# Kernel tuning notes

Hardware: AMD Instinct MI355X
Metric: run time of the kernel (lower is better)

The kernel has to match this reference:

```python
import jax, jax.numpy as jnp
import numpy as np

N = 8192        # num_drugs
D_EMB = 256     # args.gcn_hidden3 (global encoder input)
D_FEAT = 256    # args.hidden_size (local encoder input)
H1 = H2 = H3 = 256  # args.ff_hidden1/2/3
LOG2 = float(np.log(2.0))
ADJ_DENSITY = 0.01


def _ff(x, w1, b1, w2, b2, w3, b3, ws, bs):
    # FF block: 3-layer ReLU MLP + linear shortcut (FF_local / FF_global)
    h = jax.nn.relu(x @ w1 + b1)
    h = jax.nn.relu(h @ w2 + b2)
    h = jax.nn.relu(h @ w3 + b3)
    return h + x @ ws + bs


def _lin_init(k, fan_in, fan_out):
    s = 1.0 / np.sqrt(fan_in)
    kw, kb = jax.random.split(k)
    w = jax.random.uniform(kw, (fan_in, fan_out), minval=-s, maxval=s, dtype=jnp.float32)
    b = jax.random.uniform(kb, (fan_out,), minval=-s, maxval=s, dtype=jnp.float32)
    return w, b


def setup_inputs() -> dict:
    key = jax.random.key(0)
    ks = jax.random.split(key, 11)
    g_w1, g_b1 = _lin_init(ks[0], D_EMB, H1)
    g_w2, g_b2 = _lin_init(ks[1], H1, H2)
    g_w3, g_b3 = _lin_init(ks[2], H2, H3)
    g_ws, g_bs = _lin_init(ks[3], D_EMB, H3)
    l_w1, l_b1 = _lin_init(ks[4], D_FEAT, H1)
    l_w2, l_b2 = _lin_init(ks[5], H1, H2)
    l_w3, l_b3 = _lin_init(ks[6], H2, H3)
    l_ws, l_bs = _lin_init(ks[7], D_FEAT, H3)
    embeddings = jax.random.normal(ks[8], (N, D_EMB), dtype=jnp.float32)
    features = jax.random.normal(ks[9], (N, D_FEAT), dtype=jnp.float32)
    adj_tensor = (jax.random.uniform(ks[10], (N, N)) < ADJ_DENSITY).astype(jnp.float32)
    return dict(embeddings=embeddings, features=features, adj_tensor=adj_tensor,
                num_drugs=N,
                g_w1=g_w1, g_b1=g_b1, g_w2=g_w2, g_b2=g_b2, g_w3=g_w3, g_b3=g_b3,
                g_ws=g_ws, g_bs=g_bs,
                l_w1=l_w1, l_b1=l_b1, l_w2=l_w2, l_b2=l_b2, l_w3=l_w3, l_b3=l_b3,
                l_ws=l_ws, l_bs=l_bs)


def reference(embeddings, features, adj_tensor,
              g_w1, g_b1, g_w2, g_b2, g_w3, g_b3, g_ws, g_bs,
              l_w1, l_b1, l_w2, l_b2, l_w3, l_b3, l_ws, l_bs,
              num_drugs):
    g_enc = _ff(embeddings, g_w1, g_b1, g_w2, g_b2, g_w3, g_b3, g_ws, g_bs)  # [N, H3]
    l_enc = _ff(features,   l_w1, l_b1, l_w2, l_b2, l_w3, l_b3, l_ws, l_bs)  # [N, H3]
    res = l_enc @ g_enc.T                      # [N, N] pairwise local-global scores
    pos_mask = adj_tensor
    neg_mask = 1.0 - adj_tensor
    # JSD estimator (as in InfoGraph/MIRACLE: mask applied BEFORE the expectation)
    p = res * pos_mask
    E_pos = jnp.sum(LOG2 - jax.nn.softplus(-p)) / num_drugs
    q = res * neg_mask
    E_neg = jnp.sum(jax.nn.softplus(-q) + q - LOG2) / (num_drugs * (num_drugs - 1))
    return E_neg - E_pos  # prior=False -> PRIOR term is 0
```

## Files before the change

kernel.cpp:

```cpp
#include <hip/hip_runtime.h>
#include <hip/hip_bf16.h>
#include <stdint.h>

typedef __bf16 bf16;
typedef __bf16 bf16x8 __attribute__((ext_vector_type(8)));
typedef float f32x4 __attribute__((ext_vector_type(4)));

#define N_DRUGS 8192
#define DIM 256
#define LOG2_C 0.6931471805599453f
#define W_POS (1.0f / 8192.0f)
#define W_NEG (1.0f / (8192.0f * 8191.0f))

__device__ inline void gload_lds16(const void* g, void* l) {
  __builtin_amdgcn_global_load_lds(
      (const __attribute__((address_space(1))) void*)g,
      (__attribute__((address_space(3))) void*)l, 16, 0, 0);
}

__device__ inline int swz(int row, int c) {
  return (c & ~7) | ((c ^ row) & 7);
}

__device__ inline float load_as_f32(const void* p, size_t idx, int dt_bf16) {
  return dt_bf16 ? (float)((const bf16*)p)[idx] : ((const float*)p)[idx];
}

__global__ void detect_dtype(const unsigned short* emb, int* flag) {
  int l = threadIdx.x & 63;
  unsigned short u = emb[2 * l];
  int e = (u >> 7) & 0xFF;
  int plausible = (e >= 96 && e <= 140) || (u == 0);
  unsigned long long m = __ballot(plausible);
  if (l == 0) *flag = (__popcll(m) >= 32) ? 1 : 0;
}

struct P8 { const void* p[8]; };

__global__ __launch_bounds__(256) void transpose_w(P8 srcs, bf16* wt,
                                                   const int* flag) {
  __shared__ bf16 t[32][33];
  const int dt = *flag;
  int m = blockIdx.z;
  const void* src = srcs.p[m];
  bf16* dst = wt + m * 65536;
  int bx = blockIdx.x * 32;
  int by = blockIdx.y * 32;
  int tx = threadIdx.x, ty = threadIdx.y;
#pragma unroll
  for (int i = 0; i < 32; i += 8)
    t[ty + i][tx] = (bf16)load_as_f32(src, (size_t)(by + ty + i) * DIM + bx + tx, dt);
  __syncthreads();
#pragma unroll
  for (int i = 0; i < 32; i += 8)
    dst[(bx + ty + i) * DIM + by + tx] = t[tx][ty + i];
}

struct FFArgs {
  const void *x, *b1, *b2, *b3, *bs;
  const bf16 *wt1, *wt2, *wt3, *wts;
  bf16* out;
};
struct FFBoth { FFArgs a[2]; };

__global__ __launch_bounds__(512) void ff_kernel(FFBoth both, const int* flag) {
  __shared__ __align__(16) bf16 xin[64 * 256];
  __shared__ __align__(16) bf16 cur[64 * 256];
  const FFArgs A = (blockIdx.y == 0) ? both.a[0] : both.a[1];
  const int dt = *flag;

  const int t = threadIdx.x;
  const int w = t >> 6, l = t & 63;
  const int lm = l & 15, lq = l >> 4;
  const int n0 = w * 32;
  const int r0 = blockIdx.x * 64;

  if (dt) {
#pragma unroll
    for (int it = 0; it < 4; ++it) {
      int ci = it * 512 + t, row = ci >> 5, c = ci & 31;
      *(bf16x8*)&xin[row * 256 + swz(row, c) * 8] =
          *(const bf16x8*)&((const bf16*)A.x)[(size_t)(r0 + row) * DIM + c * 8];
    }
  } else {
#pragma unroll
    for (int it = 0; it < 4; ++it) {
      int ci = it * 512 + t, row = ci >> 5, c = ci & 31;
      const float* src = &((const float*)A.x)[(size_t)(r0 + row) * DIM + c * 8];
      bf16x8 v;
#pragma unroll
      for (int e = 0; e < 8; ++e) v[e] = (bf16)src[e];
      *(bf16x8*)&xin[row * 256 + swz(row, c) * 8] = v;
    }
  }
  __syncthreads();

  f32x4 acc[4][2];
  const f32x4 fz = {0.f, 0.f, 0.f, 0.f};

  auto compute = [&](const bf16* src, const bf16* wt) {
#pragma unroll
    for (int i = 0; i < 4; ++i)
#pragma unroll
      for (int j = 0; j < 2; ++j) acc[i][j] = fz;
#pragma unroll
    for (int ks = 0; ks < 256; ks += 32) {
      bf16x8 af[4], bfr[2];
#pragma unroll
      for (int i = 0; i < 4; ++i) {
        int row = i * 16 + lm;
        af[i] = *(const bf16x8*)&src[row * 256 + swz(row, (ks >> 3) + lq) * 8];
      }
#pragma unroll
      for (int j = 0; j < 2; ++j) {
        int n = n0 + j * 16 + lm;
        bfr[j] = *(const bf16x8*)&wt[n * DIM + ks + lq * 8];
      }
#pragma unroll
      for (int i = 0; i < 4; ++i)
#pragma unroll
        for (int j = 0; j < 2; ++j)
          acc[i][j] = __builtin_amdgcn_mfma_f32_16x16x32_bf16(af[i], bfr[j],
                                                              acc[i][j], 0, 0, 0);
    }
  };

  auto store_relu = [&](const void* bias) {
    __syncthreads();
#pragma unroll
    for (int j = 0; j < 2; ++j) {
      int col = n0 + j * 16 + lm;
      float bj = load_as_f32(bias, col, dt);
      int cc = col >> 3, cw = col & 7;
#pragma unroll
      for (int i = 0; i < 4; ++i)
#pragma unroll
        for (int r = 0; r < 4; ++r) {
          int row = i * 16 + lq * 4 + r;
          float v = fmaxf(acc[i][j][r] + bj, 0.f);
          cur[row * 256 + swz(row, cc) * 8 + cw] = (bf16)v;
        }
    }
    __syncthreads();
  };

  compute(xin, A.wt1); store_relu(A.b1);
  compute(cur, A.wt2); store_relu(A.b2);
  compute(cur, A.wt3); store_relu(A.b3);
  compute(xin, A.wts);

#pragma unroll
  for (int j = 0; j < 2; ++j) {
    int col = n0 + j * 16 + lm;
    float bj = load_as_f32(A.bs, col, dt);
    int cc = col >> 3, cw = col & 7;
#pragma unroll
    for (int i = 0; i < 4; ++i)
#pragma unroll
      for (int r = 0; r < 4; ++r) {
        int row = i * 16 + lq * 4 + r;
        float h3 = (float)cur[row * 256 + swz(row, cc) * 8 + cw];
        float v = acc[i][j][r] + bj + h3;
        A.out[(size_t)(r0 + row) * DIM + col] = (bf16)v;
      }
  }
}

__global__ __launch_bounds__(256) void gemm_reduce(const bf16* __restrict__ Lenc,
                                                   const bf16* __restrict__ Genc,
                                                   const void* __restrict__ adj,
                                                   float* accum, const int* flag) {
  __shared__ __align__(16) bf16 smem[2 * 128 * 64];
  __shared__ float red[8];
  bf16* At = smem;
  bf16* Bt = smem + 128 * 64;

  const int dt = *flag;
  const int t = threadIdx.x;
  const int w = t >> 6, l = t & 63;
  const int wr = w >> 1, wc = w & 1;
  const int lm = l & 15, lq = l >> 4;
  const int row0 = blockIdx.y * 128;
  const int col0 = blockIdx.x * 128;

  f32x4 acc[4][4];
  const f32x4 fz = {0.f, 0.f, 0.f, 0.f};
#pragma unroll
  for (int i = 0; i < 4; ++i)
#pragma unroll
    for (int j = 0; j < 4; ++j) acc[i][j] = fz;

  for (int kk = 0; kk < 256; kk += 64) {
    __syncthreads();
#pragma unroll
    for (int it = 0; it < 4; ++it) {
      int ci = it * 256 + t;
      int row = ci >> 3, cs = ci & 7;
      int cg = swz(row, cs);
      bf16* lbase = &At[(it * 256 + w * 64) * 8];
      gload_lds16(&Lenc[(size_t)(row0 + row) * DIM + kk + cg * 8], lbase);
      bf16* lbase2 = &Bt[(it * 256 + w * 64) * 8];
      gload_lds16(&Genc[(size_t)(col0 + row) * DIM + kk + cg * 8], lbase2);
    }
    __syncthreads();
#pragma unroll
    for (int ks = 0; ks < 64; ks += 32) {
      bf16x8 af[4], bfr[4];
#pragma unroll
      for (int i = 0; i < 4; ++i) {
        int row = wr * 64 + i * 16 + lm;
        af[i] = *(const bf16x8*)&At[row * 64 + swz(row, (ks >> 3) + lq) * 8];
      }
#pragma unroll
      for (int j = 0; j < 4; ++j) {
        int row = wc * 64 + j * 16 + lm;
        bfr[j] = *(const bf16x8*)&Bt[row * 64 + swz(row, (ks >> 3) + lq) * 8];
      }
#pragma unroll
      for (int i = 0; i < 4; ++i)
#pragma unroll
        for (int j = 0; j < 4; ++j)
          acc[i][j] = __builtin_amdgcn_mfma_f32_16x16x32_bf16(af[i], bfr[j],
                                                              acc[i][j], 0, 0, 0);
    }
  }

  float lsum = 0.f;
  __syncthreads();

  auto jsd = [&](float res, float a) {
    float s = fmaxf(res, 0.f) + __logf(1.f + __expf(-fabsf(res)));
    float vneg = (s - LOG2_C) * W_NEG;
    float vpos = (s - res - LOG2_C) * W_POS;
    return (a > 0.5f) ? vpos : vneg;
  };

  if (dt) {
    const bf16* adjB = (const bf16*)adj;
#pragma unroll
    for (int it = 0; it < 8; ++it) {
      int ci = it * 256 + t;
      int row = ci >> 4, c = ci & 15;
      int cg = c ^ (row & 15);
      bf16* lbase = &smem[(it * 256 + w * 64) * 8];
      gload_lds16(&adjB[(size_t)(row0 + row) * N_DRUGS + col0 + cg * 8], lbase);
    }
    __syncthreads();
#pragma unroll
    for (int i = 0; i < 4; ++i)
#pragma unroll
      for (int r = 0; r < 4; ++r) {
        int row = wr * 64 + i * 16 + lq * 4 + r;
#pragma unroll
        for (int j = 0; j < 4; ++j) {
          int col = wc * 64 + j * 16 + lm;
          int slot = (col >> 3) ^ (row & 15);
          float a = (float)smem[(row * 16 + slot) * 8 + (col & 7)];
          lsum += jsd(acc[i][j][r], a);
        }
      }
  } else {
    const float* adjF = (const float*)adj;
    float* AdjL = (float*)smem;
    for (int h = 0; h < 2; ++h) {
      if (h) __syncthreads();
#pragma unroll
      for (int it = 0; it < 8; ++it) {
        int ci = it * 256 + t;
        int r4 = ci >> 5, c = ci & 31;
        int pr = (r4 >> 5) * 64 + h * 32 + (r4 & 31);
        int cg = (c & 16) | ((c ^ (r4 & 15)) & 15);
        float* lbase = &AdjL[(it * 256 + w * 64) * 4];
        gload_lds16(&adjF[(size_t)(row0 + pr) * N_DRUGS + col0 + cg * 4], lbase);
      }
      __syncthreads();
#pragma unroll
      for (int ii = 0; ii < 2; ++ii) {
        int i = 2 * h + ii;
#pragma unroll
        for (int r = 0; r < 4; ++r) {
          int r4 = wr * 32 + ii * 16 + lq * 4 + r;
#pragma unroll
          for (int j = 0; j < 4; ++j) {
            int col = wc * 64 + j * 16 + lm;
            int cread = col >> 2;
            int slot = (cread & 16) | ((cread ^ (r4 & 15)) & 15);
            float a = AdjL[(r4 * 32 + slot) * 4 + (col & 3)];
            lsum += jsd(acc[i][j][r], a);
          }
        }
      }
      if (h == 0) __syncthreads();
    }
  }

#pragma unroll
  for (int off = 32; off > 0; off >>= 1) lsum += __shfl_down(lsum, off, 64);
  if (l == 0) red[w] = lsum;
  __syncthreads();
  if (t == 0) atomicAdd(accum, red[0] + red[1] + red[2] + red[3]);
}

__global__ void finalize_k(const float* accum, unsigned int* out) {
  if (threadIdx.x == 0 && blockIdx.x == 0) {
    float v = *accum;
    union { bf16 h; unsigned short u; } cv;
    cv.h = (bf16)v;
    out[0] = ((unsigned int)cv.u << 16) | cv.u;
  }
}

extern "C" void kernel_launch(void* const* d_in, const int* in_sizes, int n_in,
                              void* d_out, int out_size, void* d_ws, size_t ws_size,
                              hipStream_t stream) {
  const void* embeddings = d_in[0];
  const void* features   = d_in[1];
  const void* adj        = d_in[2];

  char* ws = (char*)d_ws;
  float* accum = (float*)ws;
  int* flag = (int*)(ws + 64);
  bf16* wt   = (bf16*)(ws + 1024);
  bf16* genc = (bf16*)(ws + 1024 + 8 * 65536 * 2);
  bf16* lenc = (bf16*)(ws + 1024 + 8 * 65536 * 2 + (size_t)N_DRUGS * DIM * 2);

  hipMemsetAsync(accum, 0, sizeof(float), stream);

  detect_dtype<<<1, 64, 0, stream>>>((const unsigned short*)embeddings, flag);

  P8 srcs;
  srcs.p[0] = d_in[4];  srcs.p[1] = d_in[6];  srcs.p[2] = d_in[8];  srcs.p[3] = d_in[10];
  srcs.p[4] = d_in[12]; srcs.p[5] = d_in[14]; srcs.p[6] = d_in[16]; srcs.p[7] = d_in[18];
  transpose_w<<<dim3(8, 8, 8), dim3(32, 8), 0, stream>>>(srcs, wt, flag);

  FFBoth fb;
  fb.a[0] = FFArgs{embeddings, d_in[5], d_in[7], d_in[9], d_in[11],
                   wt + 0 * 65536, wt + 1 * 65536, wt + 2 * 65536, wt + 3 * 65536,
                   genc};
  fb.a[1] = FFArgs{features, d_in[13], d_in[15], d_in[17], d_in[19],
                   wt + 4 * 65536, wt + 5 * 65536, wt + 6 * 65536, wt + 7 * 65536,
                   lenc};
  ff_kernel<<<dim3(128, 2), 512, 0, stream>>>(fb, flag);

  gemm_reduce<<<dim3(64, 64), 256, 0, stream>>>(lenc, genc, adj, accum, flag);

  finalize_k<<<1, 64, 0, stream>>>(accum, (unsigned int*)d_out);
}
```

Measured before the change: 451.8 us.

## Load adjacency mask directly to registers and fuse finalize via ticket counter

The GEMM epilogue now reads adjacency values straight from global memory into registers in the MFMA fragment layout, replacing the async global-to-LDS staging and its barriers. The final bf16 conversion kernel is removed: the last block to finish, found with an atomic ticket, writes the output. The FF kernel now stages its output tile in LDS and writes it out with 16-byte vector stores. The direct loads are narrower and less coalesced than the 16-byte LDS loads, which may hurt memory efficiency on the large mask read.

```diff
diff --git a/kernel.cpp b/kernel.cpp
--- a/kernel.cpp
+++ b/kernel.cpp
@@ -149,6 +149,7 @@
   compute(cur, A.wt3); store_relu(A.b3);
   compute(xin, A.wts);
 
+  __syncthreads();
 #pragma unroll
   for (int j = 0; j < 2; ++j) {
     int col = n0 + j * 16 + lm;
@@ -161,17 +162,26 @@
         int row = i * 16 + lq * 4 + r;
         float h3 = (float)cur[row * 256 + swz(row, cc) * 8 + cw];
         float v = acc[i][j][r] + bj + h3;
-        A.out[(size_t)(r0 + row) * DIM + col] = (bf16)v;
-      }
+        xin[row * 256 + swz(row, cc) * 8 + cw] = (bf16)v;
+      }
+  }
+  __syncthreads();
+#pragma unroll
+  for (int it = 0; it < 4; ++it) {
+    int ci = it * 512 + t, row = ci >> 5, c = ci & 31;
+    *(bf16x8*)&A.out[(size_t)(r0 + row) * DIM + c * 8] =
+        *(const bf16x8*)&xin[row * 256 + swz(row, c) * 8];
   }
 }
 
 __global__ __launch_bounds__(256) void gemm_reduce(const bf16* __restrict__ Lenc,
                                                    const bf16* __restrict__ Genc,
                                                    const void* __restrict__ adj,
-                                                   float* accum, const int* flag) {
+                                                   float* accum, unsigned int* ticket,
+                                                   unsigned int* out,
+                                                   const int* flag) {
   __shared__ __align__(16) bf16 smem[2 * 128 * 64];
-  __shared__ float red[8];
+  __shared__ float red[4];
   bf16* At = smem;
   bf16* Bt = smem + 128 * 64;
 
@@ -225,9 +235,6 @@
     }
   }
 
-  float lsum = 0.f;
-  __syncthreads();
-
   auto jsd = [&](float res, float a) {
     float s = fmaxf(res, 0.f) + __logf(1.f + __expf(-fabsf(res)));
     float vneg = (s - LOG2_C) * W_NEG;
@@ -235,78 +242,53 @@
     return (a > 0.5f) ? vpos : vneg;
   };
 
+  float lsum = 0.f;
+  const int rbase = row0 + wr * 64 + lq * 4;
+  const int cbase = col0 + wc * 64 + lm;
+
+  float av[4][4][4];
   if (dt) {
     const bf16* adjB = (const bf16*)adj;
 #pragma unroll
-    for (int it = 0; it < 8; ++it) {
-      int ci = it * 256 + t;
-      int row = ci >> 4, c = ci & 15;
-      int cg = c ^ (row & 15);
-      bf16* lbase = &smem[(it * 256 + w * 64) * 8];
-      gload_lds16(&adjB[(size_t)(row0 + row) * N_DRUGS + col0 + cg * 8], lbase);
-    }
-    __syncthreads();
-#pragma unroll
     for (int i = 0; i < 4; ++i)
 #pragma unroll
       for (int r = 0; r < 4; ++r) {
-        int row = wr * 64 + i * 16 + lq * 4 + r;
-#pragma unroll
-        for (int j = 0; j < 4; ++j) {
-          int col = wc * 64 + j * 16 + lm;
-          int slot = (col >> 3) ^ (row & 15);
-          float a = (float)smem[(row * 16 + slot) * 8 + (col & 7)];
-          lsum += jsd(acc[i][j][r], a);
-        }
+        const bf16* rp = adjB + (size_t)(rbase + i * 16 + r) * N_DRUGS + cbase;
+#pragma unroll
+        for (int j = 0; j < 4; ++j) av[i][r][j] = (float)rp[j * 16];
       }
   } else {
     const float* adjF = (const float*)adj;
-    float* AdjL = (float*)smem;
-    for (int h = 0; h < 2; ++h) {
-      if (h) __syncthreads();
-#pragma unroll
-      for (int it = 0; it < 8; ++it) {
-        int ci = it * 256 + t;
-        int r4 = ci >> 5, c = ci & 31;
-        int pr = (r4 >> 5) * 64 + h * 32 + (r4 & 31);
-        int cg = (c & 16) | ((c ^ (r4 & 15)) & 15);
-        float* lbase = &AdjL[(it * 256 + w * 64) * 4];
-        gload_lds16(&adjF[(size_t)(row0 + pr) * N_DRUGS + col0 + cg * 4], lbase);
-      }
-      __syncthreads();
-#pragma unroll
-      for (int ii = 0; ii < 2; ++ii) {
-        int i = 2 * h + ii;
-#pragma unroll
-        for (int r = 0; r < 4; ++r) {
-          int r4 = wr * 32 + ii * 16 + lq * 4 + r;
-#pragma unroll
-          for (int j = 0; j < 4; ++j) {
-            int col = wc * 64 + j * 16 + lm;
-            int cread = col >> 2;
-            int slot = (cread & 16) | ((cread ^ (r4 & 15)) & 15);
-            float a = AdjL[(r4 * 32 + slot) * 4 + (col & 3)];
-            lsum += jsd(acc[i][j][r], a);
-          }
-        }
-      }
-      if (h == 0) __syncthreads();
-    }
-  }
+#pragma unroll
+    for (int i = 0; i < 4; ++i)
+#pragma unroll
+      for (int r = 0; r < 4; ++r) {
+        const float* rp = adjF + (size_t)(rbase + i * 16 + r) * N_DRUGS + cbase;
+#pragma unroll
+        for (int j = 0; j < 4; ++j) av[i][r][j] = rp[j * 16];
+      }
+  }
+#pragma unroll
+  for (int i = 0; i < 4; ++i)
+#pragma unroll
+    for (int r = 0; r < 4; ++r)
+#pragma unroll
+      for (int j = 0; j < 4; ++j) lsum += jsd(acc[i][j][r], av[i][r][j]);
 
 #pragma unroll
   for (int off = 32; off > 0; off >>= 1) lsum += __shfl_down(lsum, off, 64);
   if (l == 0) red[w] = lsum;
   __syncthreads();
-  if (t == 0) atomicAdd(accum, red[0] + red[1] + red[2] + red[3]);
-}
-
-__global__ void finalize_k(const float* accum, unsigned int* out) {
-  if (threadIdx.x == 0 && blockIdx.x == 0) {
-    float v = *accum;
-    union { bf16 h; unsigned short u; } cv;
-    cv.h = (bf16)v;
-    out[0] = ((unsigned int)cv.u << 16) | cv.u;
+  if (t == 0) {
+    atomicAdd(accum, red[0] + red[1] + red[2] + red[3]);
+    __threadfence();
+    unsigned int old = atomicAdd(ticket, 1u);
+    if (old == 64u * 64u - 1u) {
+      float v = atomicAdd(accum, 0.0f);
+      union { bf16 h; unsigned short u; } cv;
+      cv.h = (bf16)v;
+      out[0] = ((unsigned int)cv.u << 16) | cv.u;
+    }
   }
 }
 
@@ -319,12 +301,13 @@
 
   char* ws = (char*)d_ws;
   float* accum = (float*)ws;
+  unsigned int* ticket = (unsigned int*)(ws + 8);
   int* flag = (int*)(ws + 64);
   bf16* wt   = (bf16*)(ws + 1024);
   bf16* genc = (bf16*)(ws + 1024 + 8 * 65536 * 2);
   bf16* lenc = (bf16*)(ws + 1024 + 8 * 65536 * 2 + (size_t)N_DRUGS * DIM * 2);
 
-  hipMemsetAsync(accum, 0, sizeof(float), stream);
+  hipMemsetAsync(ws, 0, 16, stream);
 
   detect_dtype<<<1, 64, 0, stream>>>((const unsigned short*)embeddings, flag);
 
@@ -342,7 +325,6 @@
                    lenc};
   ff_kernel<<<dim3(128, 2), 512, 0, stream>>>(fb, flag);
 
-  gemm_reduce<<<dim3(64, 64), 256, 0, stream>>>(lenc, genc, adj, accum, flag);
-
-  finalize_k<<<1, 64, 0, stream>>>(accum, (unsigned int*)d_out);
-}
+  gemm_reduce<<<dim3(64, 64), 256, 0, stream>>>(lenc, genc, adj, accum, ticket,
+                                                (unsigned int*)d_out, flag);
+}
```

New measurement: 569.4 us. +26.0%, slower.
